# Optimization experiments

Measured on AMD Instinct MI355X. Metric: run time of the kernel, lower is better.

Reference implementation:

```python
import jax, jax.numpy as jnp
import numpy as np

N, E = 100000, 1600000
NFEAT, H2, H3, H4, NCLASS = 512, 256, 256, 128, 16


def setup_inputs() -> dict:
    key = jax.random.key(0)
    ks = jax.random.split(key, 12)
    def glorot(k, shape):
        fan_in = shape[0]
        return jax.random.normal(k, shape, dtype=jnp.float32) * (1.0 / np.sqrt(fan_in))
    return {
        "x": jax.random.normal(ks[0], (N, NFEAT), dtype=jnp.float32),
        "edge_row": jax.random.randint(ks[1], (E,), 0, N, dtype=jnp.int32),
        "edge_col": jax.random.randint(ks[2], (E,), 0, N, dtype=jnp.int32),
        # positive weights ~ normalized adjacency values (scale ~1/avg_degree)
        "edge_val": jax.random.uniform(ks[3], (E,), dtype=jnp.float32) * (1.0 / 16.0),
        "W1": glorot(ks[4], (NFEAT, H2)), "b1": jnp.zeros((H2,), jnp.float32),
        "W2": glorot(ks[5], (H2, H3)),   "b2": jnp.zeros((H3,), jnp.float32),
        "W3": glorot(ks[6], (H3, H4)),   "b3": jnp.zeros((H4,), jnp.float32),
        "Wd": glorot(ks[7], (H4, NCLASS)), "bd": jnp.zeros((NCLASS,), jnp.float32),
    }


def reference(x, edge_row, edge_col, edge_val, W1, b1, W2, b2, W3, b3, Wd, bd):
    n = x.shape[0]

    def spmm(h):
        # adj @ h with adj in COO form: out[row] += val * h[col]
        return jax.ops.segment_sum(edge_val[:, None] * h[edge_col], edge_row, num_segments=n)

    # gc1 -> relu -> (dropout is identity in eval) -> gc2 -> relu -> gc3 -> relu -> dense
    h = jax.nn.relu(spmm(x @ W1) + b1)
    h = jax.nn.relu(spmm(h @ W2) + b2)
    h = jax.nn.relu(spmm(h @ W3) + b3)
    return h @ Wd + bd
```

## Files before the change

### kernel.cpp

```cpp
#include <hip/hip_runtime.h>
#include <hip/hip_bf16.h>
#include <cstdint>
#include <cstddef>

#define NFEAT 512
#define H2 256
#define H3 256
#define H4 128
#define NCLASS 16

typedef __attribute__((ext_vector_type(8))) short short8;
typedef __attribute__((ext_vector_type(4))) float f32x4;
typedef __attribute__((ext_vector_type(4))) unsigned short ushort4v;
typedef __attribute__((ext_vector_type(4))) _Float16 half4v;
typedef __attribute__((ext_vector_type(2))) _Float16 half2v;

#define AS1 __attribute__((address_space(1)))
#define AS3 __attribute__((address_space(3)))

__device__ inline unsigned short f2bf_rne(float x) {
    unsigned int u = __builtin_bit_cast(unsigned int, x);
    unsigned int r = (u + 0x7FFFu + ((u >> 16) & 1u)) >> 16;
    return (unsigned short)r;
}
__device__ inline float bf2f(unsigned short h) {
    return __builtin_bit_cast(float, (unsigned int)h << 16);
}

template <int VM> __device__ __forceinline__ void vm_wait() {
    asm volatile("s_waitcnt vmcnt(%0)" :: "n"(VM) : "memory");
}
__device__ __forceinline__ void lgkm0() {
    asm volatile("s_waitcnt lgkmcnt(0)" ::: "memory");
}

__global__ void k_hist(const int* __restrict__ er, int* __restrict__ cnt, int E) {
    for (int e = blockIdx.x * blockDim.x + threadIdx.x; e < E; e += gridDim.x * blockDim.x)
        atomicAdd(&cnt[er[e]], 1);
}

__global__ void k_scan1(const int* __restrict__ cnt, int* __restrict__ ex,
                        int* __restrict__ bsum, int n) {
    __shared__ int s[256];
    int i = blockIdx.x * 256 + threadIdx.x;
    int v = (i < n) ? cnt[i] : 0;
    s[threadIdx.x] = v;
    __syncthreads();
    #pragma unroll
    for (int off = 1; off < 256; off <<= 1) {
        int t = (threadIdx.x >= (unsigned)off) ? s[threadIdx.x - off] : 0;
        __syncthreads();
        s[threadIdx.x] += t;
        __syncthreads();
    }
    if (i < n) ex[i] = s[threadIdx.x] - v;
    if (threadIdx.x == 255) bsum[blockIdx.x] = s[255];
}

__global__ void k_scan2(int* __restrict__ bsum, int nb) {
    __shared__ int s[512];
    int v = ((int)threadIdx.x < nb) ? bsum[threadIdx.x] : 0;
    s[threadIdx.x] = v;
    __syncthreads();
    #pragma unroll
    for (int off = 1; off < 512; off <<= 1) {
        int t = (threadIdx.x >= (unsigned)off) ? s[threadIdx.x - off] : 0;
        __syncthreads();
        s[threadIdx.x] += t;
        __syncthreads();
    }
    if ((int)threadIdx.x < nb) bsum[threadIdx.x] = s[threadIdx.x] - v;
}

__global__ void k_scan3(int* __restrict__ rp, int* __restrict__ ofs,
                        const int* __restrict__ bsum, const int* __restrict__ cnt,
                        int n) {
    int i = blockIdx.x * 256 + threadIdx.x;
    if (i < n) {
        int v = rp[i] + bsum[blockIdx.x];
        rp[i] = v;
        ofs[i] = v;
        if (i == n - 1) rp[n] = v + cnt[i];
    }
}

__global__ void k_scatter_sl(const int* __restrict__ er, const int* __restrict__ ec,
                             const float* __restrict__ ev, int* __restrict__ ofs,
                             int2* __restrict__ ev2, int E, int sliceSz) {
    const int slice = blockIdx.x & 7;
    const int g = blockIdx.x >> 3;
    const int rlo = slice * sliceSz;
    const int rhi = rlo + sliceSz;
    for (int e = g * 256 + threadIdx.x; e < E; e += 256 * 256) {
        int r = er[e];
        if (r >= rlo && r < rhi) {
            int p = atomicAdd(&ofs[r], 1);
            ev2[p] = make_int2(ec[e], __builtin_bit_cast(int, ev[e]));
        }
    }
}

__global__ __launch_bounds__(256)
void k_packb(const float* __restrict__ W, unsigned short* __restrict__ hi,
             unsigned short* __restrict__ lo, int K, int M) {
    int idx = blockIdx.x * 256 + threadIdx.x;
    int NT = K >> 5;
    int total = (M >> 4) * NT * 64;
    if (idx >= total) return;
    int l = idx & 63;
    int t = (idx >> 6) % NT;
    int cg = idx / (NT << 6);
    int col = cg * 16 + (l & 15);
    int k0 = t * 32 + (l >> 4) * 8;
    short8 h8, l8;
    #pragma unroll
    for (int j = 0; j < 8; ++j) {
        float x = W[(size_t)(k0 + j) * M + col];
        unsigned short h = f2bf_rne(x);
        h8[j] = (short)h;
        l8[j] = (short)f2bf_rne(x - bf2f(h));
    }
    *(short8*)&hi[(size_t)idx * 8] = h8;
    *(short8*)&lo[(size_t)idx * 8] = l8;
}

__global__ __launch_bounds__(256, 3)
void k_gemm1c(const float* __restrict__ X, const unsigned short* __restrict__ Bh,
              const unsigned short* __restrict__ Bl, _Float16* __restrict__ C16, const int N) {
    constexpr int K = 512, M = 256, NT = K / 32;
    __shared__ char smem[24576];
    float* sX = (float*)smem;
    const int tid = threadIdx.x;
    const int lane = tid & 63;
    const int w = tid >> 6;
    const int lm = lane & 15, lk = lane >> 4;
    const int row0 = blockIdx.x * 64;
    const int col0 = w * 64;

    const int kseg = (lane & 7) ^ ((lane >> 3) & 7);
    const int r0 = min(row0 + w * 16 + (lane >> 3), N - 1);
    const int r1 = min(row0 + w * 16 + 8 + (lane >> 3), N - 1);
    const size_t ga0 = (size_t)r0 * K + kseg * 4;
    const size_t ga1 = (size_t)r1 * K + kseg * 4;

    const unsigned short* bfh = Bh + ((size_t)(w * 4) * NT) * 512 + lane * 8;
    const unsigned short* bfl = Bl + ((size_t)(w * 4) * NT) * 512 + lane * 8;

    f32x4 acc[4][4];
    #pragma unroll
    for (int i = 0; i < 4; ++i)
        #pragma unroll
        for (int j = 0; j < 4; ++j) acc[i][j] = (f32x4){0.f, 0.f, 0.f, 0.f};

    auto stage = [&](int bi, int kk) {
        __builtin_amdgcn_global_load_lds((const AS1 void*)(X + ga0 + kk),
                                         (AS3 void*)(sX + bi * 2048 + w * 512), 16, 0, 0);
        __builtin_amdgcn_global_load_lds((const AS1 void*)(X + ga1 + kk),
                                         (AS3 void*)(sX + bi * 2048 + w * 512 + 256), 16, 0, 0);
    };

    stage(0, 0); stage(1, 32); stage(2, 64);

    short8 bhf[4], blf[4];
    #pragma unroll
    for (int nf = 0; nf < 4; ++nf) {
        const size_t o = (size_t)nf * NT * 512;
        bhf[nf] = *(const short8*)(bfh + o);
        blf[nf] = *(const short8*)(bfl + o);
    }

    const int u0 = ((2 * lk) ^ (lm & 7)) * 4;
    const int u1 = ((2 * lk + 1) ^ (lm & 7)) * 4;
    int bi = 0;

#define G1_BODY(T, VM)                                                          \
    {                                                                           \
        vm_wait<VM>();                                                          \
        __builtin_amdgcn_s_barrier();                                           \
        __builtin_amdgcn_sched_barrier(0);                                      \
        short8 bhn[4], bln[4];                                                  \
        _Pragma("unroll")                                                       \
        for (int nf = 0; nf < 4; ++nf) { bhn[nf] = bhf[nf]; bln[nf] = blf[nf]; }\
        if ((T) + 1 < NT) {                                                     \
            _Pragma("unroll")                                                   \
            for (int nf = 0; nf < 4; ++nf) {                                    \
                const size_t o = ((size_t)nf * NT + (T) + 1) * 512;             \
                bhn[nf] = *(const short8*)(bfh + o);                            \
                bln[nf] = *(const short8*)(bfl + o);                            \
            }                                                                   \
        }                                                                       \
        __builtin_amdgcn_sched_barrier(0);                                      \
        _Pragma("unroll")                                                       \
        for (int mf = 0; mf < 4; ++mf) {                                        \
            const float* ab = sX + bi * 2048 + (mf * 16 + lm) * 32;             \
            f32x4 p0 = *(const f32x4*)(ab + u0);                                \
            f32x4 p1 = *(const f32x4*)(ab + u1);                                \
            float vv[8] = {p0.x, p0.y, p0.z, p0.w, p1.x, p1.y, p1.z, p1.w};     \
            short8 ah, al;                                                      \
            _Pragma("unroll")                                                   \
            for (int j = 0; j < 8; ++j) {                                       \
                unsigned int uu = __builtin_bit_cast(unsigned int, vv[j]);      \
                ah[j] = (short)(uu >> 16);                                      \
                float hi_ = __builtin_bit_cast(float, uu & 0xFFFF0000u);        \
                al[j] = (short)f2bf_rne(vv[j] - hi_);                           \
            }                                                                   \
            _Pragma("unroll")                                                   \
            for (int nf = 0; nf < 4; ++nf) {                                    \
                acc[mf][nf] = __builtin_amdgcn_mfma_f32_16x16x32_bf16(ah, bhf[nf], acc[mf][nf], 0, 0, 0); \
                acc[mf][nf] = __builtin_amdgcn_mfma_f32_16x16x32_bf16(ah, blf[nf], acc[mf][nf], 0, 0, 0); \
                acc[mf][nf] = __builtin_amdgcn_mfma_f32_16x16x32_bf16(al, bhf[nf], acc[mf][nf], 0, 0, 0); \
            }                                                                   \
        }                                                                       \
        lgkm0();                                                                \
        __builtin_amdgcn_sched_barrier(0);                                      \
        __builtin_amdgcn_s_barrier();                                           \
        if ((T) + 3 < NT) stage(bi, ((T) + 3) * 32);                            \
        _Pragma("unroll")                                                       \
        for (int nf = 0; nf < 4; ++nf) { bhf[nf] = bhn[nf]; blf[nf] = bln[nf]; }\
        bi = bi + 1; if (bi == 3) bi = 0;                                       \
    }

    for (int t = 0; t < NT - 2; ++t) G1_BODY(t, 12);
    G1_BODY(NT - 2, 10);
    G1_BODY(NT - 1, 8);
#undef G1_BODY

    float* sc = (float*)smem;
    #pragma unroll
    for (int mf = 0; mf < 4; ++mf) {
        __syncthreads();
        #pragma unroll
        for (int nf = 0; nf < 4; ++nf)
            #pragma unroll
            for (int r = 0; r < 4; ++r) {
                const int rl = lk * 4 + r;
                const int col = col0 + nf * 16 + lm;
                sc[rl * M + (col ^ (lk << 3))] = acc[mf][nf][r];
            }
        __syncthreads();
        #pragma unroll
        for (int i = 0; i < 4; ++i) {
            const int idx = i * 256 + tid;
            const int rl = idx >> 6, u = idx & 63;
            const int grow = row0 + mf * 16 + rl;
            if (grow < N) {
                f32x4 v = *(const f32x4*)&sc[rl * M + ((u * 4) ^ (((rl >> 2) & 3) << 3))];
                half4v h;
                h[0] = (_Float16)v[0]; h[1] = (_Float16)v[1];
                h[2] = (_Float16)v[2]; h[3] = (_Float16)v[3];
                *(half4v*)&C16[(size_t)grow * M + u * 4] = h;
            }
        }
    }
}

template <int K, int NFW>
__global__ __launch_bounds__(256, 3)
void k_gemm_btc(const unsigned short* __restrict__ Ah, const unsigned short* __restrict__ Al,
                const unsigned short* __restrict__ Bh, const unsigned short* __restrict__ Bl,
                _Float16* __restrict__ C16, const int N) {
    constexpr int M = 64 * NFW;
    constexpr int NT = K / 32;
    constexpr int UPR = 16 * NFW;
    __shared__ char smem[24576];
    unsigned short* sAh = (unsigned short*)smem;
    unsigned short* sAl = sAh + 6144;
    const int tid = threadIdx.x;
    const int lane = tid & 63;
    const int w = tid >> 6;
    const int lm = lane & 15, lk = lane >> 4;
    const int row0 = blockIdx.x * 64;
    const int col0 = w * (16 * NFW);

    const int kseg = (lane & 3) ^ ((lane >> 2) & 3);
    const int gr = min(row0 + w * 16 + (lane >> 2), N - 1);
    const size_t ga = (size_t)gr * K + kseg * 8;

    const int aoff = lm * 32 + ((lk ^ (lm & 3)) * 8);

    const unsigned short* bfh = Bh + ((size_t)(w * NFW) * NT) * 512 + lane * 8;
    const unsigned short* bfl = Bl + ((size_t)(w * NFW) * NT) * 512 + lane * 8;

    f32x4 acc[4][NFW];
    #pragma unroll
    for (int i = 0; i < 4; ++i)
        #pragma unroll
        for (int j = 0; j < NFW; ++j) acc[i][j] = (f32x4){0.f, 0.f, 0.f, 0.f};

    auto stage = [&](int bi, int kk) {
        __builtin_amdgcn_global_load_lds((const AS1 void*)(Ah + ga + kk),
                                         (AS3 void*)(sAh + bi * 2048 + w * 512), 16, 0, 0);
        __builtin_amdgcn_global_load_lds((const AS1 void*)(Al + ga + kk),
                                         (AS3 void*)(sAl + bi * 2048 + w * 512), 16, 0, 0);
    };

    stage(0, 0); stage(1, 32); stage(2, 64);

    short8 bhf[NFW], blf[NFW];
    #pragma unroll
    for (int nf = 0; nf < NFW; ++nf) {
        const size_t o = (size_t)nf * NT * 512;
        bhf[nf] = *(const short8*)(bfh + o);
        blf[nf] = *(const short8*)(bfl + o);
    }

    int bi = 0;

#define GBT_BODY(T, VM)                                                         \
    {                                                                           \
        vm_wait<VM>();                                                          \
        __builtin_amdgcn_s_barrier();                                           \
        __builtin_amdgcn_sched_barrier(0);                                      \
        short8 bhn[NFW], bln[NFW];                                              \
        _Pragma("unroll")                                                       \
        for (int nf = 0; nf < NFW; ++nf) { bhn[nf] = bhf[nf]; bln[nf] = blf[nf]; } \
        if ((T) + 1 < NT) {                                                     \
            _Pragma("unroll")                                                   \
            for (int nf = 0; nf < NFW; ++nf) {                                  \
                const size_t o = ((size_t)nf * NT + (T) + 1) * 512;             \
                bhn[nf] = *(const short8*)(bfh + o);                            \
                bln[nf] = *(const short8*)(bfl + o);                            \
            }                                                                   \
        }                                                                       \
        __builtin_amdgcn_sched_barrier(0);                                      \
        _Pragma("unroll")                                                       \
        for (int mf = 0; mf < 4; ++mf) {                                        \
            short8 ah = *(const short8*)&sAh[bi * 2048 + aoff + mf * 512];      \
            short8 al = *(const short8*)&sAl[bi * 2048 + aoff + mf * 512];      \
            _Pragma("unroll")                                                   \
            for (int nf = 0; nf < NFW; ++nf) {                                  \
                acc[mf][nf] = __builtin_amdgcn_mfma_f32_16x16x32_bf16(ah, bhf[nf], acc[mf][nf], 0, 0, 0); \
                acc[mf][nf] = __builtin_amdgcn_mfma_f32_16x16x32_bf16(ah, blf[nf], acc[mf][nf], 0, 0, 0); \
                acc[mf][nf] = __builtin_amdgcn_mfma_f32_16x16x32_bf16(al, bhf[nf], acc[mf][nf], 0, 0, 0); \
            }                                                                   \
        }                                                                       \
        lgkm0();                                                                \
        __builtin_amdgcn_sched_barrier(0);                                      \
        __builtin_amdgcn_s_barrier();                                           \
        if ((T) + 3 < NT) stage(bi, ((T) + 3) * 32);                            \
        _Pragma("unroll")                                                       \
        for (int nf = 0; nf < NFW; ++nf) { bhf[nf] = bhn[nf]; blf[nf] = bln[nf]; } \
        bi = bi + 1; if (bi == 3) bi = 0;                                       \
    }

    for (int t = 0; t < NT - 2; ++t) GBT_BODY(t, 2 * NFW + 4);
    GBT_BODY(NT - 2, 2 * NFW + 2);
    GBT_BODY(NT - 1, 2 * NFW);
#undef GBT_BODY

    float* sc = (float*)smem;
    #pragma unroll
    for (int mf = 0; mf < 4; ++mf) {
        __syncthreads();
        #pragma unroll
        for (int nf = 0; nf < NFW; ++nf)
            #pragma unroll
            for (int r = 0; r < 4; ++r) {
                const int rl = lk * 4 + r;
                const int col = col0 + nf * 16 + lm;
                sc[rl * M + (col ^ (lk << 3))] = acc[mf][nf][r];
            }
        __syncthreads();
        #pragma unroll
        for (int i = 0; i < (16 * UPR) / 256; ++i) {
            const int idx = i * 256 + tid;
            const int rl = idx / UPR, u = idx % UPR;
            const int grow = row0 + mf * 16 + rl;
            if (grow < N) {
                f32x4 v = *(const f32x4*)&sc[rl * M + ((u * 4) ^ (((rl >> 2) & 3) << 3))];
                half4v h;
                h[0] = (_Float16)v[0]; h[1] = (_Float16)v[1];
                h[2] = (_Float16)v[2]; h[3] = (_Float16)v[3];
                *(half4v*)&C16[(size_t)grow * M + u * 4] = h;
            }
        }
    }
}

__global__ __launch_bounds__(256)
void k_spmm256f(const int* __restrict__ rp, const int2* __restrict__ ev2,
                const _Float16* __restrict__ in16, const float* __restrict__ bias,
                unsigned short* __restrict__ oh, unsigned short* __restrict__ ol, int N) {
    const int lane = threadIdx.x & 63;
    int r = __builtin_amdgcn_readfirstlane(blockIdx.x * 4 + (threadIdx.x >> 6));
    if (r >= N) return;
    const int e0 = __builtin_amdgcn_readfirstlane(rp[r]);
    const int e1 = __builtin_amdgcn_readfirstlane(rp[r + 1]);
    f32x4 acc = {0.f, 0.f, 0.f, 0.f};
    const _Float16* base = in16 + lane * 4;

    #pragma unroll 4
    for (int e = e0; e < e1; ++e) {
        int2 p = ev2[e];
        half4v hv = *(const half4v*)(base + (size_t)p.x * 256);
        float val = __builtin_bit_cast(float, p.y);
        acc[0] = fmaf(val, (float)hv[0], acc[0]);
        acc[1] = fmaf(val, (float)hv[1], acc[1]);
        acc[2] = fmaf(val, (float)hv[2], acc[2]);
        acc[3] = fmaf(val, (float)hv[3], acc[3]);
    }

    f32x4 bv = *(const f32x4*)&bias[lane * 4];
    ushort4v h, l;
    #pragma unroll
    for (int j = 0; j < 4; ++j) {
        float o = fmaxf(acc[j] + bv[j], 0.f);
        unsigned short hh = f2bf_rne(o);
        h[j] = hh;
        l[j] = f2bf_rne(o - bf2f(hh));
    }
    *(ushort4v*)&oh[(size_t)r * 256 + lane * 4] = h;
    *(ushort4v*)&ol[(size_t)r * 256 + lane * 4] = l;
}

__global__ __launch_bounds__(256)
void k_spmm128f(const int* __restrict__ rp, const int2* __restrict__ ev2,
                const _Float16* __restrict__ in16, const float* __restrict__ b3,
                const float* __restrict__ Wd, const float* __restrict__ bd,
                float* __restrict__ out, int N) {
    __shared__ float Ws[H4 * NCLASS];
    __shared__ float hrow[4][H4];
    {
        int i = threadIdx.x * 8;
        *(f32x4*)&Ws[i] = *(const f32x4*)&Wd[i];
        *(f32x4*)&Ws[i + 4] = *(const f32x4*)&Wd[i + 4];
    }
    __syncthreads();

    const int lane = threadIdx.x & 63;
    const int w = threadIdx.x >> 6;
    int r = __builtin_amdgcn_readfirstlane(blockIdx.x * 4 + w);
    if (r >= N) return;
    const int e0 = __builtin_amdgcn_readfirstlane(rp[r]);
    const int e1 = __builtin_amdgcn_readfirstlane(rp[r + 1]);
    float a0 = 0.f, a1 = 0.f;
    const _Float16* base = in16 + lane * 2;

    #pragma unroll 4
    for (int e = e0; e < e1; ++e) {
        int2 p = ev2[e];
        half2v hv = *(const half2v*)(base + (size_t)p.x * 128);
        float v = __builtin_bit_cast(float, p.y);
        a0 = fmaf(v, (float)hv[0], a0);
        a1 = fmaf(v, (float)hv[1], a1);
    }

    float2 hb;
    hb.x = fmaxf(a0 + b3[lane * 2 + 0], 0.f);
    hb.y = fmaxf(a1 + b3[lane * 2 + 1], 0.f);
    *(float2*)&hrow[w][lane * 2] = hb;

    const int c = lane & 15, q = lane >> 4;
    float s = 0.f;
    #pragma unroll
    for (int k = q * 32; k < q * 32 + 32; ++k)
        s = fmaf(hrow[w][k], Ws[k * NCLASS + c], s);
    s += __shfl_xor(s, 16);
    s += __shfl_xor(s, 32);
    if (lane < 16) out[(size_t)r * NCLASS + lane] = s + bd[lane];
}

extern "C" void kernel_launch(void* const* d_in, const int* in_sizes, int n_in,
                              void* d_out, int out_size, void* d_ws, size_t ws_size,
                              hipStream_t stream) {
    const float* x  = (const float*)d_in[0];
    const int*   er = (const int*)d_in[1];
    const int*   ec = (const int*)d_in[2];
    const float* ev = (const float*)d_in[3];
    const float* W1 = (const float*)d_in[4];
    const float* b1 = (const float*)d_in[5];
    const float* W2 = (const float*)d_in[6];
    const float* b2 = (const float*)d_in[7];
    const float* W3 = (const float*)d_in[8];
    const float* b3 = (const float*)d_in[9];
    const float* Wd = (const float*)d_in[10];
    const float* bd = (const float*)d_in[11];
    float* out = (float*)d_out;

    const int N = in_sizes[0] / NFEAT;
    const int E = in_sizes[1];

    char* w = (char*)d_ws;
    auto alloc = [&](size_t bytes) { char* p = w; w += (bytes + 255) & ~(size_t)255; return p; };
    _Float16* C16 = (_Float16*)alloc((size_t)N * 256 * 2);
    unsigned short* hh = (unsigned short*)alloc((size_t)N * 256 * 2);
    unsigned short* hl = (unsigned short*)alloc((size_t)N * 256 * 2);
    int* cnt  = (int*)alloc((size_t)N * 4);
    int* rp   = (int*)alloc((size_t)(N + 1) * 4);
    int* ofs  = (int*)alloc((size_t)N * 4);
    int2* ev2 = (int2*)alloc((size_t)E * 8);
    int* bsum = (int*)alloc(4096);
    unsigned short* W1h = (unsigned short*)alloc((size_t)NFEAT * H2 * 2);
    unsigned short* W1l = (unsigned short*)alloc((size_t)NFEAT * H2 * 2);
    unsigned short* W2h = (unsigned short*)alloc((size_t)H2 * H3 * 2);
    unsigned short* W2l = (unsigned short*)alloc((size_t)H2 * H3 * 2);
    unsigned short* W3h = (unsigned short*)alloc((size_t)H3 * H4 * 2);
    unsigned short* W3l = (unsigned short*)alloc((size_t)H3 * H4 * 2);

    const int nb = (N + 255) / 256;
    const int sliceSz = (N + 7) / 8;

    hipMemsetAsync(cnt, 0, (size_t)N * 4, stream);
    k_hist<<<1024, 256, 0, stream>>>(er, cnt, E);
    k_scan1<<<nb, 256, 0, stream>>>(cnt, rp, bsum, N);
    k_scan2<<<1, 512, 0, stream>>>(bsum, nb);
    k_scan3<<<nb, 256, 0, stream>>>(rp, ofs, bsum, cnt, N);
    k_scatter_sl<<<2048, 256, 0, stream>>>(er, ec, ev, ofs, ev2, E, sliceSz);

    k_packb<<<(NFEAT * H2 / 8 + 255) / 256, 256, 0, stream>>>(W1, W1h, W1l, NFEAT, H2);
    k_packb<<<(H2 * H3 / 8 + 255) / 256, 256, 0, stream>>>(W2, W2h, W2l, H2, H3);
    k_packb<<<(H3 * H4 / 8 + 255) / 256, 256, 0, stream>>>(W3, W3h, W3l, H3, H4);

    const int rgrid = (N + 63) / 64;
    const int sgrid = (N + 3) / 4;

    k_gemm1c<<<rgrid, 256, 0, stream>>>(x, W1h, W1l, C16, N);
    k_spmm256f<<<sgrid, 256, 0, stream>>>(rp, ev2, C16, b1, hh, hl, N);

    k_gemm_btc<H2, 4><<<rgrid, 256, 0, stream>>>(hh, hl, W2h, W2l, C16, N);
    k_spmm256f<<<sgrid, 256, 0, stream>>>(rp, ev2, C16, b2, hh, hl, N);

    k_gemm_btc<H3, 2><<<rgrid, 256, 0, stream>>>(hh, hl, W3h, W3l, C16, N);
    k_spmm128f<<<sgrid, 256, 0, stream>>>(rp, ev2, C16, b3, Wd, bd, out, N);
}
```

Baseline: 665.1 us.

## Convert X tile to bf16 hi/lo once per block into shared double buffer

In the first GEMM, each wave previously split fp32 X values into bf16 hi/lo pairs for every fragment it read, so the conversion was repeated across all four waves. Now each tile is converted once per block into dedicated bf16 hi/lo shared-memory buffers, and the next tile's conversion is overlapped with the current tile's MFMAs. The MFMA loop then reads pre-split operands directly. This raises shared memory from 24 KB to 40 KB per block, which may reduce occupancy, and adds extra LDS writes plus a tighter vm_wait schedule.

```diff
diff --git a/kernel.cpp b/kernel.cpp
--- a/kernel.cpp
+++ b/kernel.cpp
@@ -125,11 +125,13 @@
 }
 
 __global__ __launch_bounds__(256, 3)
-void k_gemm1c(const float* __restrict__ X, const unsigned short* __restrict__ Bh,
+void k_gemm1d(const float* __restrict__ X, const unsigned short* __restrict__ Bh,
               const unsigned short* __restrict__ Bl, _Float16* __restrict__ C16, const int N) {
     constexpr int K = 512, M = 256, NT = K / 32;
-    __shared__ char smem[24576];
-    float* sX = (float*)smem;
+    __shared__ char smem[40960];
+    float* sXf = (float*)smem;
+    unsigned short* sAh = (unsigned short*)(smem + 24576);
+    unsigned short* sAl = (unsigned short*)(smem + 32768);
     const int tid = threadIdx.x;
     const int lane = tid & 63;
     const int w = tid >> 6;
@@ -143,8 +145,15 @@
     const size_t ga0 = (size_t)r0 * K + kseg * 4;
     const size_t ga1 = (size_t)r1 * K + kseg * 4;
 
+    const int crow = w * 16 + (lane >> 2);
+    const int ch = lane & 3;
+    const int cu0 = ((2 * ch) ^ (crow & 7)) * 4;
+    const int cu1 = ((2 * ch + 1) ^ (crow & 7)) * 4;
+    const int cwo = crow * 32 + (ch ^ (crow & 3)) * 8;
+
     const unsigned short* bfh = Bh + ((size_t)(w * 4) * NT) * 512 + lane * 8;
     const unsigned short* bfl = Bl + ((size_t)(w * 4) * NT) * 512 + lane * 8;
+    const int aoff = lm * 32 + ((lk ^ (lm & 3)) * 8);
 
     f32x4 acc[4][4];
     #pragma unroll
@@ -154,13 +163,29 @@
 
     auto stage = [&](int bi, int kk) {
         __builtin_amdgcn_global_load_lds((const AS1 void*)(X + ga0 + kk),
-                                         (AS3 void*)(sX + bi * 2048 + w * 512), 16, 0, 0);
+                                         (AS3 void*)(sXf + bi * 2048 + w * 512), 16, 0, 0);
         __builtin_amdgcn_global_load_lds((const AS1 void*)(X + ga1 + kk),
-                                         (AS3 void*)(sX + bi * 2048 + w * 512 + 256), 16, 0, 0);
+                                         (AS3 void*)(sXf + bi * 2048 + w * 512 + 256), 16, 0, 0);
     };
 
+    auto convert = [&](int src, int dst) {
+        const float* s = sXf + src * 2048 + crow * 32;
+        f32x4 p0 = *(const f32x4*)(s + cu0);
+        f32x4 p1 = *(const f32x4*)(s + cu1);
+        float vv[8] = {p0.x, p0.y, p0.z, p0.w, p1.x, p1.y, p1.z, p1.w};
+        short8 ah, al;
+        #pragma unroll
+        for (int j = 0; j < 8; ++j) {
+            unsigned int uu = __builtin_bit_cast(unsigned int, vv[j]);
+            ah[j] = (short)(uu >> 16);
+            float hi_ = __builtin_bit_cast(float, uu & 0xFFFF0000u);
+            al[j] = (short)f2bf_rne(vv[j] - hi_);
+        }
+        *(short8*)&sAh[dst * 2048 + cwo] = ah;
+        *(short8*)&sAl[dst * 2048 + cwo] = al;
+    };
+
     stage(0, 0); stage(1, 32); stage(2, 64);
-
     short8 bhf[4], blf[4];
     #pragma unroll
     for (int nf = 0; nf < 4; ++nf) {
@@ -168,12 +193,14 @@
         bhf[nf] = *(const short8*)(bfh + o);
         blf[nf] = *(const short8*)(bfl + o);
     }
-
-    const int u0 = ((2 * lk) ^ (lm & 7)) * 4;
-    const int u1 = ((2 * lk + 1) ^ (lm & 7)) * 4;
-    int bi = 0;
-
-#define G1_BODY(T, VM)                                                          \
+    vm_wait<12>();
+    convert(0, 0);
+    lgkm0();
+    __builtin_amdgcn_s_barrier();
+
+    int b0 = 0;
+
+#define G1D_BODY(T, VM)                                                         \
     {                                                                           \
         vm_wait<VM>();                                                          \
         __builtin_amdgcn_s_barrier();                                           \
@@ -192,18 +219,8 @@
         __builtin_amdgcn_sched_barrier(0);                                      \
         _Pragma("unroll")                                                       \
         for (int mf = 0; mf < 4; ++mf) {                                        \
-            const float* ab = sX + bi * 2048 + (mf * 16 + lm) * 32;             \
-            f32x4 p0 = *(const f32x4*)(ab + u0);                                \
-            f32x4 p1 = *(const f32x4*)(ab + u1);                                \
-            float vv[8] = {p0.x, p0.y, p0.z, p0.w, p1.x, p1.y, p1.z, p1.w};     \
-            short8 ah, al;                                                      \
-            _Pragma("unroll")                                                   \
-            for (int j = 0; j < 8; ++j) {                                       \
-                unsigned int uu = __builtin_bit_cast(unsigned int, vv[j]);      \
-                ah[j] = (short)(uu >> 16);                                      \
-                float hi_ = __builtin_bit_cast(float, uu & 0xFFFF0000u);        \
-                al[j] = (short)f2bf_rne(vv[j] - hi_);                           \
-            }                                                                   \
+            short8 ah = *(const short8*)&sAh[((T) & 1) * 2048 + aoff + mf * 512]; \
+            short8 al = *(const short8*)&sAl[((T) & 1) * 2048 + aoff + mf * 512]; \
             _Pragma("unroll")                                                   \
             for (int nf = 0; nf < 4; ++nf) {                                    \
                 acc[mf][nf] = __builtin_amdgcn_mfma_f32_16x16x32_bf16(ah, bhf[nf], acc[mf][nf], 0, 0, 0); \
@@ -211,19 +228,23 @@
                 acc[mf][nf] = __builtin_amdgcn_mfma_f32_16x16x32_bf16(al, bhf[nf], acc[mf][nf], 0, 0, 0); \
             }                                                                   \
         }                                                                       \
+        if ((T) + 1 < NT) {                                                     \
+            int src = b0 + 1; if (src == 3) src = 0;                            \
+            convert(src, ((T) + 1) & 1);                                        \
+        }                                                                       \
         lgkm0();                                                                \
         __builtin_amdgcn_sched_barrier(0);                                      \
         __builtin_amdgcn_s_barrier();                                           \
-        if ((T) + 3 < NT) stage(bi, ((T) + 3) * 32);                            \
+        if ((T) + 3 < NT) stage(b0, ((T) + 3) * 32);                            \
         _Pragma("unroll")                                                       \
         for (int nf = 0; nf < 4; ++nf) { bhf[nf] = bhn[nf]; blf[nf] = bln[nf]; }\
-        bi = bi + 1; if (bi == 3) bi = 0;                                       \
-    }
-
-    for (int t = 0; t < NT - 2; ++t) G1_BODY(t, 12);
-    G1_BODY(NT - 2, 10);
-    G1_BODY(NT - 1, 8);
-#undef G1_BODY
+        b0 = b0 + 1; if (b0 == 3) b0 = 0;                                       \
+    }
+
+    for (int t = 0; t < NT - 2; ++t) G1D_BODY(t, 10);
+    G1D_BODY(NT - 2, 8);
+    G1D_BODY(NT - 1, 8);
+#undef G1D_BODY
 
     float* sc = (float*)smem;
     #pragma unroll
@@ -514,7 +535,7 @@
     const int rgrid = (N + 63) / 64;
     const int sgrid = (N + 3) / 4;
 
-    k_gemm1c<<<rgrid, 256, 0, stream>>>(x, W1h, W1l, C16, N);
+    k_gemm1d<<<rgrid, 256, 0, stream>>>(x, W1h, W1l, C16, N);
     k_spmm256f<<<sgrid, 256, 0, stream>>>(rp, ev2, C16, b1, hh, hl, N);
 
     k_gemm_btc<H2, 4><<<rgrid, 256, 0, stream>>>(hh, hl, W2h, W2l, C16, N);
```

Result: no change. 656.1 us (-1.4%).
